# Kernel tuning notes

Measured on AMD Instinct MI355X. Metric: run time of the kernel, lower is better.

Reference implementation:

```python
import jax, jax.numpy as jnp
import numpy as np

B, S, D, H = 2, 4096, 512, 8
HD = D // H

def setup_inputs() -> dict:
    key = jax.random.key(0)
    ks = jax.random.split(key, 11)
    s = 1.0 / np.sqrt(D)
    return {
        "x": jax.random.normal(ks[0], (B, S, D), jnp.float32),
        "y": jax.random.normal(ks[1], (B, S, D), jnp.float32),
        "z": jax.random.normal(ks[2], (B, S, D), jnp.float32),
        "Wq": jax.random.normal(ks[3], (D, D), jnp.float32) * s,
        "bq": jnp.zeros((D,), jnp.float32),
        "Wk": jax.random.normal(ks[4], (D, D), jnp.float32) * s,
        "bk": jnp.zeros((D,), jnp.float32),
        "Wv": jax.random.normal(ks[5], (D, D), jnp.float32) * s,
        "bv": jnp.zeros((D,), jnp.float32),
        "Wp": jax.random.normal(ks[6], (D, D), jnp.float32) * s,
        "bp": jnp.zeros((D,), jnp.float32),
    }

def reference(x, y, z, Wq, bq, Wk, bk, Wv, bv, Wp, bp):
    # q/k/v projections, split heads: [B,S,D] -> [B,H,S,HD]
    def heads(t):
        return t.reshape(B, -1, H, HD).transpose(0, 2, 1, 3)
    q = heads(x @ Wq + bq)
    k = heads(y @ Wk + bk)
    v = heads(z @ Wv + bv)
    att = jnp.einsum('bhqd,bhkd->bhqk', q, k) / np.sqrt(HD).astype(np.float32)
    att = jax.nn.softmax(att, axis=-1)  # dropout is identity in eval mode
    out = jnp.einsum('bhqk,bhkd->bhqd', att, v)
    out = out.transpose(0, 2, 1, 3).reshape(B, -1, D)
    return out @ Wp + bp
```

## Files before the change

### kernel.cpp

```cpp
#include <hip/hip_runtime.h>
#include <math.h>

#define B_ 2
#define S_ 4096
#define D_ 512
#define H_ 8
#define HD_ 64
#define NROW_ (B_ * S_)
#define NELEM_ ((size_t)NROW_ * D_)
#define WELEM_ ((size_t)D_ * D_)

#define LOG2E_ 1.44269504f
#define SCLAMP_ 15.869645f

typedef _Float16 half8 __attribute__((ext_vector_type(8)));
typedef _Float16 half4v __attribute__((ext_vector_type(4)));
typedef __fp16 fp16x2 __attribute__((ext_vector_type(2)));
typedef float floatx4 __attribute__((ext_vector_type(4)));
typedef float floatx16 __attribute__((ext_vector_type(16)));
typedef int intx2 __attribute__((ext_vector_type(2)));
typedef unsigned uintx4 __attribute__((ext_vector_type(4)));

__device__ __forceinline__ half8 cvt_half8(float4 a, float4 b) {
  fp16x2 l0 = __builtin_amdgcn_cvt_pkrtz(a.x, a.y);
  fp16x2 l1 = __builtin_amdgcn_cvt_pkrtz(a.z, a.w);
  fp16x2 l2 = __builtin_amdgcn_cvt_pkrtz(b.x, b.y);
  fp16x2 l3 = __builtin_amdgcn_cvt_pkrtz(b.z, b.w);
  half8 h;
  h[0] = l0[0]; h[1] = l0[1]; h[2] = l1[0]; h[3] = l1[1];
  h[4] = l2[0]; h[5] = l2[1]; h[6] = l3[0]; h[7] = l3[1];
  return h;
}

__device__ __forceinline__ void permswap32(unsigned& a, unsigned& b) {
#if __has_builtin(__builtin_amdgcn_permlane32_swap)
  intx2 r = __builtin_amdgcn_permlane32_swap((int)a, (int)b, false, false);
  a = (unsigned)r[0];
  b = (unsigned)r[1];
#else
  asm volatile("v_permlane32_swap_b32 %0, %1" : "+v"(a), "+v"(b));
#endif
}

__device__ __forceinline__ float exp2_hw(float x) {
  float r;
  asm("v_exp_f32 %0, %1" : "=v"(r) : "v"(x));
  return r;
}

typedef const unsigned __attribute__((address_space(1))) gu32_t;
typedef unsigned __attribute__((address_space(3))) lu32_t;
__device__ __forceinline__ void gload16(const void* g, void* l) {
  __builtin_amdgcn_global_load_lds((gu32_t*)g, (lu32_t*)l, 16, 0, 0);
}

struct PrepPtrs { const float *W0, *W1, *W2, *W3, *X0, *X1; };

__global__ __launch_bounds__(256) void prep_kernel(
    PrepPtrs p, _Float16* __restrict__ WTbase, _Float16* __restrict__ Xh) {
  __shared__ float tl[32][33];
  const int bid = blockIdx.x;
  const int t = threadIdx.x;
  if (bid < 1024) {
    const int z = bid >> 8, r8 = bid & 255;
    const int bx = r8 & 15, by = r8 >> 4;
    const float* W = z == 0 ? p.W0 : z == 1 ? p.W1 : z == 2 ? p.W2 : p.W3;
    const float scale = z == 0 ? 0.125f * LOG2E_ : 1.0f;
    _Float16* Wt = WTbase + (size_t)z * WELEM_;
    const int k0 = by * 32, n0 = bx * 32;
    const int r = t >> 3, c0 = (t & 7) * 4;
    const float4 v = *(const float4*)&W[(size_t)(k0 + r) * D_ + n0 + c0];
    tl[r][c0 + 0] = v.x; tl[r][c0 + 1] = v.y;
    tl[r][c0 + 2] = v.z; tl[r][c0 + 3] = v.w;
    __syncthreads();
    half4v hv;
#pragma unroll
    for (int j = 0; j < 4; ++j) hv[j] = (_Float16)(tl[c0 + j][r] * scale);
    *(half4v*)&Wt[(size_t)(n0 + r) * D_ + k0 + c0] = hv;
  } else {
    const int cid = bid - 1024;
    const size_t e0 = (size_t)cid * 8192;
    const float* src = e0 < NELEM_ ? p.X0 + e0 : p.X1 + (e0 - NELEM_);
    _Float16* dst = Xh + e0;
    const float4* s4 = (const float4*)src;
#pragma unroll
    for (int j = 0; j < 4; ++j) {
      const int i8 = j * 256 + t;
      const float4 a = s4[2 * i8];
      const float4 b = s4[2 * i8 + 1];
      *(half8*)&dst[(size_t)i8 * 8] = cvt_half8(a, b);
    }
  }
}

template <bool AF16, int OUTMODE, int BM, bool GL>
__device__ __forceinline__ void gemm_body(
    const void* __restrict__ Av, const _Float16* __restrict__ Bt,
    const float* __restrict__ bias, void* __restrict__ Cout, float bscale,
    _Float16* pool, int bx, int by, int tid) {
  constexpr int MT = BM / 32;
  const int w = tid >> 6, lane = tid & 63;
  const int m = lane & 15, quad = lane >> 4;
  const int row0 = by * BM, col0 = bx * 128;
  const int wr = (w >> 1) * (BM / 2), wc = (w & 1) * 64;

  const _Float16* A16 = (const _Float16*)Av;
  const float* A32 = (const float*)Av;

  floatx4 acc[MT][4];
#pragma unroll
  for (int i = 0; i < MT; ++i)
#pragma unroll
    for (int j = 0; j < 4; ++j) acc[i][j] = floatx4{0.f, 0.f, 0.f, 0.f};

  if constexpr (GL) {
    _Float16 (*Asl)[64] = (_Float16 (*)[64])pool;
    _Float16 (*Bsl)[64] = (_Float16 (*)[64])(pool + BM * 64);
    for (int kt = 0; kt < D_ / 64; ++kt) {
      if (kt) __syncthreads();
      const int kc = kt * 64;
#pragma unroll
      for (int i = 0; i < BM / 32; ++i) {
        const int rb = (i * 4 + w) * 8;
        const int row = rb + (lane >> 3);
        const int slot = (lane & 7) ^ (row & 7);
        gload16(&A16[(size_t)(row0 + row) * D_ + kc + slot * 8], &Asl[rb][0]);
      }
#pragma unroll
      for (int i = 0; i < 4; ++i) {
        const int rb = (i * 4 + w) * 8;
        const int row = rb + (lane >> 3);
        const int slot = (lane & 7) ^ (row & 7);
        gload16(&Bt[(size_t)(col0 + row) * D_ + kc + slot * 8], &Bsl[rb][0]);
      }
      __syncthreads();
#pragma unroll
      for (int h = 0; h < 2; ++h) {
        half8 af[MT], bf[4];
#pragma unroll
        for (int mt = 0; mt < MT; ++mt) {
          const int r = wr + mt * 16 + m;
          af[mt] = *(const half8*)&Asl[r][(((4 * h + quad) ^ (r & 7)) * 8)];
        }
#pragma unroll
        for (int nt = 0; nt < 4; ++nt) {
          const int r = wc + nt * 16 + m;
          bf[nt] = *(const half8*)&Bsl[r][(((4 * h + quad) ^ (r & 7)) * 8)];
        }
#pragma unroll
        for (int mt = 0; mt < MT; ++mt)
#pragma unroll
          for (int nt = 0; nt < 4; ++nt)
            acc[mt][nt] = __builtin_amdgcn_mfma_f32_16x16x32_f16(
                af[mt], bf[nt], acc[mt][nt], 0, 0, 0);
      }
    }
  } else {
    _Float16 (*As)[72] = (_Float16 (*)[72])pool;
    _Float16 (*Bs)[72] = (_Float16 (*)[72])(pool + BM * 72);
    const int srow = tid >> 3, soff = (tid & 7) * 8;

    half8 pa16[MT];
    float4 pa32[MT][2];
    half8 pb[4];
#pragma unroll
    for (int i = 0; i < MT; ++i) {
      const size_t ar = (size_t)(row0 + srow + 32 * i) * D_ + soff;
      if (AF16) pa16[i] = *(const half8*)&A16[ar];
      else { pa32[i][0] = *(const float4*)&A32[ar];
             pa32[i][1] = *(const float4*)&A32[ar + 4]; }
    }
#pragma unroll
    for (int i = 0; i < 4; ++i)
      pb[i] = *(const half8*)&Bt[(size_t)(col0 + srow + 32 * i) * D_ + soff];

    for (int kt = 0; kt < D_ / 64; ++kt) {
      if (kt) __syncthreads();
#pragma unroll
      for (int i = 0; i < MT; ++i)
        *(half8*)&As[srow + 32 * i][soff] =
            AF16 ? pa16[i] : cvt_half8(pa32[i][0], pa32[i][1]);
#pragma unroll
      for (int i = 0; i < 4; ++i) *(half8*)&Bs[srow + 32 * i][soff] = pb[i];
      __syncthreads();
      if (kt < D_ / 64 - 1) {
        const int kc = (kt + 1) * 64 + soff;
#pragma unroll
        for (int i = 0; i < MT; ++i) {
          const size_t ar = (size_t)(row0 + srow + 32 * i) * D_ + kc;
          if (AF16) pa16[i] = *(const half8*)&A16[ar];
          else { pa32[i][0] = *(const float4*)&A32[ar];
                 pa32[i][1] = *(const float4*)&A32[ar + 4]; }
        }
#pragma unroll
        for (int i = 0; i < 4; ++i)
          pb[i] = *(const half8*)&Bt[(size_t)(col0 + srow + 32 * i) * D_ + kc];
      }
#pragma unroll
      for (int h = 0; h < 2; ++h) {
        half8 af[MT], bf[4];
#pragma unroll
        for (int mt = 0; mt < MT; ++mt)
          af[mt] = *(const half8*)&As[wr + mt * 16 + m][h * 32 + quad * 8];
#pragma unroll
        for (int nt = 0; nt < 4; ++nt)
          bf[nt] = *(const half8*)&Bs[wc + nt * 16 + m][h * 32 + quad * 8];
#pragma unroll
        for (int mt = 0; mt < MT; ++mt)
#pragma unroll
          for (int nt = 0; nt < 4; ++nt)
            acc[mt][nt] = __builtin_amdgcn_mfma_f32_16x16x32_f16(
                af[mt], bf[nt], acc[mt][nt], 0, 0, 0);
      }
    }
  }

  float bv[4];
#pragma unroll
  for (int nt = 0; nt < 4; ++nt)
    bv[nt] = bias[col0 + wc + nt * 16 + m] * bscale;

  if constexpr (OUTMODE == 2) {
    __syncthreads();
    _Float16 (*Ct)[132] = (_Float16 (*)[132])pool;
#pragma unroll
    for (int mt = 0; mt < MT; ++mt)
#pragma unroll
      for (int nt = 0; nt < 4; ++nt)
#pragma unroll
        for (int r = 0; r < 4; ++r)
          Ct[wr + mt * 16 + quad * 4 + r][wc + nt * 16 + m] =
              (_Float16)(acc[mt][nt][r] + bv[nt]);
    __syncthreads();
    const int c = tid & 127, sc = tid >> 7;
    const int head = (col0 + c) >> 6, dd = (col0 + c) & 63;
    const int b = row0 >> 12;
    const int sbase = (row0 & (S_ - 1)) + sc * 64;
    _Float16* dst = (_Float16*)Cout +
        ((size_t)(b * H_ + head) * HD_ + dd) * S_ + sbase;
#pragma unroll
    for (int j = 0; j < 8; ++j) {
      half8 o;
#pragma unroll
      for (int e = 0; e < 8; ++e) o[e] = Ct[sc * 64 + j * 8 + e][c];
      *(half8*)&dst[j * 8] = o;
    }
  } else {
#pragma unroll
    for (int mt = 0; mt < MT; ++mt)
#pragma unroll
      for (int nt = 0; nt < 4; ++nt)
#pragma unroll
        for (int r = 0; r < 4; ++r) {
          const int row = row0 + wr + mt * 16 + quad * 4 + r;
          const int col = col0 + wc + nt * 16 + m;
          const float vout = acc[mt][nt][r] + bv[nt];
          if (OUTMODE == 1)
            ((_Float16*)Cout)[(size_t)row * D_ + col] = (_Float16)vout;
          else
            ((float*)Cout)[(size_t)row * D_ + col] = vout;
        }
  }
}

struct QkvPtrs { const float *A2, *b0, *b1, *b2; };

__global__ __launch_bounds__(256, 3) void qkv_gemm_kernel(
    QkvPtrs p, const _Float16* __restrict__ WT, _Float16* __restrict__ Cb,
    _Float16* __restrict__ VhT, const _Float16* __restrict__ Xh) {
  __shared__ alignas(16) _Float16 pool[(128 + 128) * 72];
  const int z = blockIdx.z;
  if (z == 2)
    gemm_body<false, 2, 128, false>(p.A2, WT + 2 * WELEM_, p.b2, VhT, 1.0f,
                                    pool, blockIdx.x, blockIdx.y, threadIdx.x);
  else
    gemm_body<true, 1, 128, true>(Xh + (size_t)z * NELEM_,
                                  WT + (size_t)z * WELEM_,
                                  z == 0 ? p.b0 : p.b1, Cb + (size_t)z * NELEM_,
                                  z == 0 ? 0.125f * LOG2E_ : 1.0f, pool,
                                  blockIdx.x, blockIdx.y, threadIdx.x);
}

__global__ __launch_bounds__(256, 4) void out_gemm_kernel(
    const _Float16* __restrict__ Oh, const _Float16* __restrict__ WpT,
    const float* __restrict__ bp, float* __restrict__ out) {
  __shared__ alignas(16) _Float16 pool[(32 + 128) * 72];
  gemm_body<true, 0, 32, true>(Oh, WpT, bp, out, 1.0f, pool, blockIdx.x,
                               blockIdx.y, threadIdx.x);
}

__global__ __launch_bounds__(512, 4) void attn_mfma_kernel(
    const _Float16* __restrict__ Qg, const _Float16* __restrict__ Kg,
    const _Float16* __restrict__ VT, _Float16* __restrict__ Og) {
  __shared__ alignas(16) unsigned char smem[73728];
  _Float16 (*Ks)[2][64][72] =
      reinterpret_cast<_Float16 (*)[2][64][72]>(smem);
  _Float16 (*Vt)[2][64][72] =
      reinterpret_cast<_Float16 (*)[2][64][72]>(smem + 36864);
  float (*comb)[64][36] = (float (*)[64][36])smem;

  const int t = threadIdx.x;
  const int w = t >> 6;
  const int g = w >> 2;
  const int wq = w & 3;
  const int lane = t & 63;
  const int li = lane & 31;
  const int hl = lane >> 5;
  const int q0 = blockIdx.x * 128 + wq * 32;
  const int koff = g * (S_ / 2);
  const size_t base =
      (size_t)blockIdx.z * ((size_t)S_ * D_) + (size_t)blockIdx.y * HD_;
  const size_t vbase = (size_t)(blockIdx.z * H_ + blockIdx.y) * HD_ * S_;

  half8 qb[4];
#pragma unroll
  for (int ks = 0; ks < 4; ++ks)
    qb[ks] = *(const half8*)
        &Qg[base + (size_t)(q0 + li) * D_ + ks * 16 + hl * 8];

  floatx16 oacc[2];
#pragma unroll
  for (int i = 0; i < 16; ++i) { oacc[0][i] = 0.f; oacc[1][i] = 0.f; }
  float lpart = 0.f;

  const int tg = t & 255;
  const int srow = tg >> 3, soff = (tg & 7) * 8;

#pragma unroll
  for (int i = 0; i < 2; ++i) {
    *(half8*)&Ks[g][0][srow + 32 * i][soff] = *(const half8*)
        &Kg[base + (size_t)(koff + srow + 32 * i) * D_ + soff];
    *(half8*)&Vt[g][0][srow + 32 * i][soff] = *(const half8*)
        &VT[vbase + (size_t)(srow + 32 * i) * S_ + koff + soff];
  }
  half8 pk[2], pv[2];
#pragma unroll
  for (int i = 0; i < 2; ++i) {
    pk[i] = *(const half8*)
        &Kg[base + (size_t)(koff + 64 + srow + 32 * i) * D_ + soff];
    pv[i] = *(const half8*)
        &VT[vbase + (size_t)(srow + 32 * i) * S_ + koff + 64 + soff];
  }
  __syncthreads();

  constexpr int NT2 = S_ / 128;
  for (int kt = 0; kt < NT2; ++kt) {
    const int cur = kt & 1;
    if (kt + 1 < NT2) {
#pragma unroll
      for (int i = 0; i < 2; ++i) {
        *(half8*)&Ks[g][cur ^ 1][srow + 32 * i][soff] = pk[i];
        *(half8*)&Vt[g][cur ^ 1][srow + 32 * i][soff] = pv[i];
      }
      if (kt + 2 < NT2) {
        const int k2 = koff + (kt + 2) * 64;
#pragma unroll
        for (int i = 0; i < 2; ++i) {
          pk[i] = *(const half8*)
              &Kg[base + (size_t)(k2 + srow + 32 * i) * D_ + soff];
          pv[i] = *(const half8*)
              &VT[vbase + (size_t)(srow + 32 * i) * S_ + k2 + soff];
        }
      }
    }

    floatx16 sacc[2];
#pragma unroll
    for (int i = 0; i < 16; ++i) { sacc[0][i] = 0.f; sacc[1][i] = 0.f; }
    __builtin_amdgcn_s_setprio(1);
#pragma unroll
    for (int ks = 0; ks < 4; ++ks) {
      const half8 ka0 = *(const half8*)&Ks[g][cur][li][ks * 16 + hl * 8];
      const half8 ka1 = *(const half8*)&Ks[g][cur][32 + li][ks * 16 + hl * 8];
      sacc[0] = __builtin_amdgcn_mfma_f32_32x32x16_f16(ka0, qb[ks],
                                                       sacc[0], 0, 0, 0);
      sacc[1] = __builtin_amdgcn_mfma_f32_32x32x16_f16(ka1, qb[ks],
                                                       sacc[1], 0, 0, 0);
    }
    __builtin_amdgcn_s_setprio(0);

#pragma unroll
    for (int kt2 = 0; kt2 < 2; ++kt2) {
      unsigned dq[4][2];
#pragma unroll
      for (int rq = 0; rq < 4; ++rq)
#pragma unroll
        for (int pp = 0; pp < 2; ++pp) {
          const float e0 =
              exp2_hw(fminf(sacc[kt2][4 * rq + 2 * pp], SCLAMP_));
          const float e1 =
              exp2_hw(fminf(sacc[kt2][4 * rq + 2 * pp + 1], SCLAMP_));
          lpart += e0 + e1;
          const fp16x2 h2 = __builtin_amdgcn_cvt_pkrtz(e0, e1);
          dq[rq][pp] = __builtin_bit_cast(unsigned, h2);
        }
      half8 pf[2];
#pragma unroll
      for (int t2 = 0; t2 < 2; ++t2) {
        unsigned a0 = dq[2 * t2][0], b0 = dq[2 * t2 + 1][0];
        unsigned a1 = dq[2 * t2][1], b1 = dq[2 * t2 + 1][1];
        permswap32(a0, b0);
        permswap32(a1, b1);
        uintx4 u; u[0] = a0; u[1] = a1; u[2] = b0; u[3] = b1;
        pf[t2] = __builtin_bit_cast(half8, u);
      }
      __builtin_amdgcn_s_setprio(1);
#pragma unroll
      for (int t2 = 0; t2 < 2; ++t2) {
        const int ks = 2 * kt2 + t2;
        const half8 va0 = *(const half8*)&Vt[g][cur][li][ks * 16 + hl * 8];
        const half8 va1 =
            *(const half8*)&Vt[g][cur][32 + li][ks * 16 + hl * 8];
        oacc[0] = __builtin_amdgcn_mfma_f32_32x32x16_f16(va0, pf[t2],
                                                         oacc[0], 0, 0, 0);
        oacc[1] = __builtin_amdgcn_mfma_f32_32x32x16_f16(va1, pf[t2],
                                                         oacc[1], 0, 0, 0);
      }
      __builtin_amdgcn_s_setprio(0);
    }

    __syncthreads();
  }

  const float wsum = lpart + __shfl_xor(lpart, 32);

  if (g == 1) {
#pragma unroll
    for (int n = 0; n < 2; ++n)
#pragma unroll
      for (int c = 0; c < 4; ++c) {
        float4 f;
        f.x = oacc[n][4 * c + 0]; f.y = oacc[n][4 * c + 1];
        f.z = oacc[n][4 * c + 2]; f.w = oacc[n][4 * c + 3];
        *(float4*)&comb[wq][lane][n * 16 + 4 * c] = f;
      }
    comb[wq][lane][32] = wsum;
  }
  __syncthreads();
  if (g == 0) {
    const float linv = 1.0f / (wsum + comb[wq][lane][32]);
#pragma unroll
    for (int n = 0; n < 2; ++n)
#pragma unroll
      for (int rq = 0; rq < 4; ++rq) {
        const float4 cf = *(const float4*)&comb[wq][lane][n * 16 + 4 * rq];
        half4v o4;
        o4[0] = (_Float16)((oacc[n][4 * rq + 0] + cf.x) * linv);
        o4[1] = (_Float16)((oacc[n][4 * rq + 1] + cf.y) * linv);
        o4[2] = (_Float16)((oacc[n][4 * rq + 2] + cf.z) * linv);
        o4[3] = (_Float16)((oacc[n][4 * rq + 3] + cf.w) * linv);
        *(half4v*)&Og[base + (size_t)(q0 + li) * D_ +
                      n * 32 + 8 * rq + 4 * hl] = o4;
      }
  }
}

extern "C" void kernel_launch(void* const* d_in, const int* in_sizes, int n_in,
                              void* d_out, int out_size, void* d_ws,
                              size_t ws_size, hipStream_t stream) {
  const float* x  = (const float*)d_in[0];
  const float* y  = (const float*)d_in[1];
  const float* z  = (const float*)d_in[2];
  const float* Wq = (const float*)d_in[3];
  const float* bq = (const float*)d_in[4];
  const float* Wk = (const float*)d_in[5];
  const float* bk = (const float*)d_in[6];
  const float* Wv = (const float*)d_in[7];
  const float* bv = (const float*)d_in[8];
  const float* Wp = (const float*)d_in[9];
  const float* bp = (const float*)d_in[10];

  _Float16* hws = (_Float16*)d_ws;
  _Float16* WT  = hws;
  _Float16* Xh  = WT + 4 * WELEM_;
  _Float16* Qh  = Xh + 2 * NELEM_;
  _Float16* Kh  = Qh + NELEM_;
  _Float16* VhT = Kh + NELEM_;
  _Float16* Oh  = Xh;

  PrepPtrs pp{Wq, Wk, Wv, Wp, x, y};
  prep_kernel<<<dim3(2048), 256, 0, stream>>>(pp, WT, Xh);

  QkvPtrs qp{z, bq, bk, bv};
  qkv_gemm_kernel<<<dim3(4, 64, 3), 256, 0, stream>>>(qp, WT, Qh, VhT, Xh);

  attn_mfma_kernel<<<dim3(S_ / 128, H_, B_), 512, 0, stream>>>(Qh, Kh, VhT, Oh);

  out_gemm_kernel<<<dim3(4, 256), 256, 0, stream>>>(Oh, WT + 3 * WELEM_, bp,
                                                    (float*)d_out);
}
```

Before: 236.4 us.

## Software-pipeline QK^T of next tile with softmax/PV of current tile

Restructures the attention inner loop so the QK^T MFMAs for tile t+1 are issued before the exp/softmax and PV MFMAs for tile t, using two score register sets (sA/sB) and a two-way unrolled loop. This lets matrix-core work overlap with the transcendental and pack/permute VALU work. It also replaces the fp32 row-sum accumulation with an fdot2 on the packed fp16 probabilities. The changes add an extra barrier per tile and raise register pressure. Summing the fp16-rounded values slightly changes the normalizer.

```diff
diff --git a/kernel.cpp b/kernel.cpp
--- a/kernel.cpp
+++ b/kernel.cpp
@@ -15,6 +15,7 @@
 
 typedef _Float16 half8 __attribute__((ext_vector_type(8)));
 typedef _Float16 half4v __attribute__((ext_vector_type(4)));
+typedef _Float16 half2v __attribute__((ext_vector_type(2)));
 typedef __fp16 fp16x2 __attribute__((ext_vector_type(2)));
 typedef float floatx4 __attribute__((ext_vector_type(4)));
 typedef float floatx16 __attribute__((ext_vector_type(16)));
@@ -322,63 +323,46 @@
 #pragma unroll
   for (int i = 0; i < 16; ++i) { oacc[0][i] = 0.f; oacc[1][i] = 0.f; }
   float lpart = 0.f;
+  const half2v one2 = {(_Float16)1.0f, (_Float16)1.0f};
 
   const int tg = t & 255;
   const int srow = tg >> 3, soff = (tg & 7) * 8;
 
-#pragma unroll
-  for (int i = 0; i < 2; ++i) {
-    *(half8*)&Ks[g][0][srow + 32 * i][soff] = *(const half8*)
-        &Kg[base + (size_t)(koff + srow + 32 * i) * D_ + soff];
-    *(half8*)&Vt[g][0][srow + 32 * i][soff] = *(const half8*)
-        &VT[vbase + (size_t)(srow + 32 * i) * S_ + koff + soff];
-  }
   half8 pk[2], pv[2];
-#pragma unroll
-  for (int i = 0; i < 2; ++i) {
-    pk[i] = *(const half8*)
-        &Kg[base + (size_t)(koff + 64 + srow + 32 * i) * D_ + soff];
-    pv[i] = *(const half8*)
-        &VT[vbase + (size_t)(srow + 32 * i) * S_ + koff + 64 + soff];
-  }
-  __syncthreads();
-
-  constexpr int NT2 = S_ / 128;
-  for (int kt = 0; kt < NT2; ++kt) {
-    const int cur = kt & 1;
-    if (kt + 1 < NT2) {
-#pragma unroll
-      for (int i = 0; i < 2; ++i) {
-        *(half8*)&Ks[g][cur ^ 1][srow + 32 * i][soff] = pk[i];
-        *(half8*)&Vt[g][cur ^ 1][srow + 32 * i][soff] = pv[i];
-      }
-      if (kt + 2 < NT2) {
-        const int k2 = koff + (kt + 2) * 64;
-#pragma unroll
-        for (int i = 0; i < 2; ++i) {
-          pk[i] = *(const half8*)
-              &Kg[base + (size_t)(k2 + srow + 32 * i) * D_ + soff];
-          pv[i] = *(const half8*)
-              &VT[vbase + (size_t)(srow + 32 * i) * S_ + k2 + soff];
-        }
-      }
-    }
-
-    floatx16 sacc[2];
-#pragma unroll
-    for (int i = 0; i < 16; ++i) { sacc[0][i] = 0.f; sacc[1][i] = 0.f; }
+
+  auto load_regs = [&](int tile) {
+    const int k2 = koff + tile * 64;
+#pragma unroll
+    for (int i = 0; i < 2; ++i) {
+      pk[i] = *(const half8*)
+          &Kg[base + (size_t)(k2 + srow + 32 * i) * D_ + soff];
+      pv[i] = *(const half8*)
+          &VT[vbase + (size_t)(srow + 32 * i) * S_ + k2 + soff];
+    }
+  };
+  auto stage_regs = [&](int buf) {
+#pragma unroll
+    for (int i = 0; i < 2; ++i) {
+      *(half8*)&Ks[g][buf][srow + 32 * i][soff] = pk[i];
+      *(half8*)&Vt[g][buf][srow + 32 * i][soff] = pv[i];
+    }
+  };
+  auto qk_tile = [&](floatx16 (&s)[2], int buf) {
+#pragma unroll
+    for (int i = 0; i < 16; ++i) { s[0][i] = 0.f; s[1][i] = 0.f; }
     __builtin_amdgcn_s_setprio(1);
 #pragma unroll
     for (int ks = 0; ks < 4; ++ks) {
-      const half8 ka0 = *(const half8*)&Ks[g][cur][li][ks * 16 + hl * 8];
-      const half8 ka1 = *(const half8*)&Ks[g][cur][32 + li][ks * 16 + hl * 8];
-      sacc[0] = __builtin_amdgcn_mfma_f32_32x32x16_f16(ka0, qb[ks],
-                                                       sacc[0], 0, 0, 0);
-      sacc[1] = __builtin_amdgcn_mfma_f32_32x32x16_f16(ka1, qb[ks],
-                                                       sacc[1], 0, 0, 0);
+      const half8 ka0 = *(const half8*)&Ks[g][buf][li][ks * 16 + hl * 8];
+      const half8 ka1 = *(const half8*)&Ks[g][buf][32 + li][ks * 16 + hl * 8];
+      s[0] = __builtin_amdgcn_mfma_f32_32x32x16_f16(ka0, qb[ks], s[0],
+                                                    0, 0, 0);
+      s[1] = __builtin_amdgcn_mfma_f32_32x32x16_f16(ka1, qb[ks], s[1],
+                                                    0, 0, 0);
     }
     __builtin_amdgcn_s_setprio(0);
-
+  };
+  auto smpv_tile = [&](floatx16 (&s)[2], int buf) {
 #pragma unroll
     for (int kt2 = 0; kt2 < 2; ++kt2) {
       unsigned dq[4][2];
@@ -386,12 +370,16 @@
       for (int rq = 0; rq < 4; ++rq)
 #pragma unroll
         for (int pp = 0; pp < 2; ++pp) {
-          const float e0 =
-              exp2_hw(fminf(sacc[kt2][4 * rq + 2 * pp], SCLAMP_));
+          const float e0 = exp2_hw(fminf(s[kt2][4 * rq + 2 * pp], SCLAMP_));
           const float e1 =
-              exp2_hw(fminf(sacc[kt2][4 * rq + 2 * pp + 1], SCLAMP_));
+              exp2_hw(fminf(s[kt2][4 * rq + 2 * pp + 1], SCLAMP_));
+          const fp16x2 h2 = __builtin_amdgcn_cvt_pkrtz(e0, e1);
+#if __has_builtin(__builtin_amdgcn_fdot2)
+          lpart = __builtin_amdgcn_fdot2(__builtin_bit_cast(half2v, h2),
+                                         one2, lpart, false);
+#else
           lpart += e0 + e1;
-          const fp16x2 h2 = __builtin_amdgcn_cvt_pkrtz(e0, e1);
+#endif
           dq[rq][pp] = __builtin_bit_cast(unsigned, h2);
         }
       half8 pf[2];
@@ -408,9 +396,9 @@
 #pragma unroll
       for (int t2 = 0; t2 < 2; ++t2) {
         const int ks = 2 * kt2 + t2;
-        const half8 va0 = *(const half8*)&Vt[g][cur][li][ks * 16 + hl * 8];
+        const half8 va0 = *(const half8*)&Vt[g][buf][li][ks * 16 + hl * 8];
         const half8 va1 =
-            *(const half8*)&Vt[g][cur][32 + li][ks * 16 + hl * 8];
+            *(const half8*)&Vt[g][buf][32 + li][ks * 16 + hl * 8];
         oacc[0] = __builtin_amdgcn_mfma_f32_32x32x16_f16(va0, pf[t2],
                                                          oacc[0], 0, 0, 0);
         oacc[1] = __builtin_amdgcn_mfma_f32_32x32x16_f16(va1, pf[t2],
@@ -418,8 +406,45 @@
       }
       __builtin_amdgcn_s_setprio(0);
     }
-
-    __syncthreads();
+  };
+
+#pragma unroll
+  for (int i = 0; i < 2; ++i) {
+    *(half8*)&Ks[g][0][srow + 32 * i][soff] = *(const half8*)
+        &Kg[base + (size_t)(koff + srow + 32 * i) * D_ + soff];
+    *(half8*)&Vt[g][0][srow + 32 * i][soff] = *(const half8*)
+        &VT[vbase + (size_t)(srow + 32 * i) * S_ + koff + soff];
+  }
+  load_regs(1);
+  __syncthreads();
+
+  floatx16 sA[2], sB[2];
+  qk_tile(sA, 0);
+
+  constexpr int NT2 = S_ / 128;
+  for (int kt = 0; kt < NT2; kt += 2) {
+    {
+      const int tt = kt;
+      if (tt + 1 < NT2) {
+        stage_regs(1);
+        __syncthreads();
+        qk_tile(sB, 1);
+        if (tt + 2 < NT2) load_regs(tt + 2);
+      }
+      smpv_tile(sA, 0);
+      __syncthreads();
+    }
+    {
+      const int tt = kt + 1;
+      if (tt + 1 < NT2) {
+        stage_regs(0);
+        __syncthreads();
+        qk_tile(sA, 0);
+        if (tt + 2 < NT2) load_regs(tt + 2);
+      }
+      smpv_tile(sB, 1);
+      __syncthreads();
+    }
   }
 
   const float wsum = lpart + __shfl_xor(lpart, 32);
```

New measurement: 416.3 us. +76.1%, slower.
